# Optimization experiments

Measured on AMD Instinct MI355X. Metric: run time of the kernel, lower is better.

The kernel has to match this reference:

```python
import jax, jax.numpy as jnp
import numpy as np

B, D_IN, D_H = 16384, 512, 1024


def _glorot(key, out_d, in_d):
    lim = 1.0 / np.sqrt(in_d)
    return jax.random.uniform(key, (out_d, in_d), minval=-lim, maxval=lim, dtype=jnp.float32)


def setup_inputs() -> dict:
    key = jax.random.key(0)
    ks = jax.random.split(key, 16)
    inp = {
        "x_t": jax.random.normal(ks[0], (B, D_IN), dtype=jnp.float32),
        "delta_t": jax.random.uniform(ks[1], (B, 1), dtype=jnp.float32),
        "h_prev": jax.random.normal(ks[2], (B, D_H), dtype=jnp.float32),
        # torch nn.Linear weights are [out, in]; y = x @ W.T
        "W_sh": _glorot(ks[3], D_H, D_H),
        "W_sx": _glorot(ks[4], D_H, D_IN),
        "W_st": _glorot(ks[5], D_H, 1),
        "b_s": jnp.zeros((D_H,), jnp.float32),
        "WTh": _glorot(ks[6], D_H, D_H),
        "WTx": _glorot(ks[7], D_H, D_IN),
        "WTs": _glorot(ks[8], D_H, D_H),
        "b_T": jnp.zeros((D_H,), jnp.float32),
        "W_rh": _glorot(ks[9], D_H, D_H),
        "W_rx": _glorot(ks[10], D_H, D_IN),
        "b_r": jnp.zeros((D_H,), jnp.float32),
        "W_zh": _glorot(ks[11], D_H, D_H),
        "W_zx": _glorot(ks[12], D_H, D_IN),
        "b_z": jnp.zeros((D_H,), jnp.float32),
        "W_h": _glorot(ks[13], D_H, D_H),
        "W_x": _glorot(ks[14], D_H, D_IN),
        "b": jnp.zeros((D_H,), jnp.float32),
    }
    return inp


def reference(x_t, delta_t, h_prev,
              W_sh, W_sx, W_st, b_s,
              WTh, WTx, WTs, b_T,
              W_rh, W_rx, b_r,
              W_zh, W_zx, b_z,
              W_h, W_x, b):
    lin = lambda x, W: x @ W.T  # nn.Linear(bias=False)
    s_t = jnp.tanh(lin(h_prev, W_sh) + lin(x_t, W_sx) + lin(delta_t, W_st) + b_s)
    T_t = jax.nn.sigmoid(lin(h_prev, WTh) + lin(x_t, WTx) + lin(s_t, WTs) + b_T)
    r_t = jax.nn.sigmoid(lin(h_prev, W_rh) + lin(x_t, W_rx) + b_r)
    z_t = jax.nn.sigmoid(lin(h_prev, W_zh) + lin(x_t, W_zx) + b_z)
    h_tilde = jnp.tanh(lin(r_t * h_prev, W_h) + lin(x_t, W_x) + b)
    h_t = (1.0 - z_t) * (T_t * h_prev) + z_t * h_tilde
    return h_t
```

## Files before the change

kernel.cpp:

```cpp
#include <hip/hip_runtime.h>
#include <stdint.h>

#define AS1 __attribute__((address_space(1)))
#define AS3 __attribute__((address_space(3)))

typedef unsigned short US;
typedef __bf16 bf16x8 __attribute__((ext_vector_type(8)));
typedef float f32x4 __attribute__((ext_vector_type(4)));
typedef int intx4 __attribute__((ext_vector_type(4)));

static constexpr int Bsz = 16384;
static constexpr int DIN = 512;
static constexpr int DH  = 1024;
static constexpr int LDA = 2560;
static constexpr int LDR = 1536;

__device__ __forceinline__ US f2bf(float f) {
  unsigned u = __float_as_uint(f);
  u += 0x7fffu + ((u >> 16) & 1u);
  return (US)(u >> 16);
}
__device__ __forceinline__ float bf2f(US u) { return __uint_as_float(((unsigned)u) << 16); }
__device__ __forceinline__ float sigm(float x) { return 1.f / (1.f + __expf(-x)); }
__device__ __forceinline__ float tanh_f(float x) { return 1.f - 2.f / (1.f + __expf(2.f * x)); }

__device__ __forceinline__ intx4 dsr128(unsigned addr) {
  intx4 r;
  asm volatile("ds_read_b128 %0, %1" : "=v"(r) : "v"(addr));
  return r;
}

#define SBAR  asm volatile("s_barrier")
#define SB0   __builtin_amdgcn_sched_barrier(0)
#define LGKM0 { asm volatile("s_waitcnt lgkmcnt(0)"); __builtin_amdgcn_sched_barrier(0); }

__global__ void pack_A(const float* __restrict__ h, const float* __restrict__ x,
                       US* __restrict__ Ab, US* __restrict__ RHx) {
  const int total = Bsz * 384;
  for (int idx = blockIdx.x * blockDim.x + threadIdx.x; idx < total;
       idx += gridDim.x * blockDim.x) {
    int row = idx / 384;
    int c = (idx - row * 384) * 4;
    const float* src = (c < DH) ? (h + (size_t)row * DH + c)
                                : (x + (size_t)row * DIN + (c - DH));
    float4 v = *(const float4*)src;
    ushort4 o;
    o.x = f2bf(v.x); o.y = f2bf(v.y); o.z = f2bf(v.z); o.w = f2bf(v.w);
    *(ushort4*)(Ab + (size_t)row * LDA + c) = o;
    if (c >= DH) *(ushort4*)(RHx + (size_t)row * LDR + c) = o;
  }
}

struct WSlot { const float* src; US* dst; int n4; int ksh; int ld; int co; };
struct WBatch { WSlot s[11]; };
__global__ void conv_w(WBatch b) {
  WSlot sl = b.s[blockIdx.y];
  const int mask = (1 << sl.ksh) - 1;
  for (int i = blockIdx.x * blockDim.x + threadIdx.x; i < sl.n4;
       i += gridDim.x * blockDim.x) {
    float4 v = *(const float4*)(sl.src + (size_t)i * 4);
    ushort4 o;
    o.x = f2bf(v.x); o.y = f2bf(v.y); o.z = f2bf(v.z); o.w = f2bf(v.w);
    int r = i >> sl.ksh;
    int cc = (i & mask) * 4;
    *(ushort4*)(sl.dst + (size_t)r * sl.ld + sl.co + cc) = o;
  }
}

template <int EPI, int NBLK>
__global__ __launch_bounds__(512, 2) void gemm8(
    const US* __restrict__ A, int lda,
    const US* __restrict__ W, int ldw, int nt,
    const float* __restrict__ bias0, const float* __restrict__ bias1,
    const float* __restrict__ bias2,
    const void* aux0, const void* aux1, const void* aux2,
    void* out0, int ldo0, void* out1, void* out2) {
  __shared__ __align__(16) US As[2][256 * 64];
  __shared__ __align__(16) US Bs[2][256 * 64];

  const int tid  = threadIdx.x;
  const int lane = tid & 63;
  const int w    = tid >> 6;
  const int wr   = w >> 2;
  const int wc   = w & 3;
  const int quad = lane >> 4, l15 = lane & 15;
  const int sw8  = l15 & 7;
  const int lrow = lane >> 3;
  const int scc  = (lane & 7) ^ (lrow & 7);

  const int p = blockIdx.x;
  const int c = p & 7, q = p >> 3;
  const int nIdx = q % NBLK, mIdx = c * 8 + q / NBLK;
  const int mBase = mIdx * 256, nBase = nIdx * 256;

  f32x4 acc[8][4];
#pragma unroll
  for (int i = 0; i < 8; i++)
#pragma unroll
    for (int j = 0; j < 4; j++) acc[i][j] = f32x4{0.f, 0.f, 0.f, 0.f};

  const unsigned aBase = (unsigned)(uintptr_t)&As[0][0];
  const unsigned bBase = (unsigned)(uintptr_t)&Bs[0][0];
  const unsigned arB = (unsigned)((wr * 128 + l15) * 128);
  const unsigned brB = (unsigned)((wc * 64 + l15) * 128);
  const unsigned kc0 = (unsigned)((quad ^ sw8) * 16);

  const size_t aRowS = (size_t)(mBase + w * 8 + lrow) * lda;
  const size_t wRowS = (size_t)(nBase + w * 8 + lrow) * ldw;
  const int sccOff = scc * 8;

#define STAGE_A(d, hh, co)                                                       \
  { const US* g = A + aRowS + (size_t)(hh) * 128 * lda + (co) + sccOff;          \
    __builtin_amdgcn_global_load_lds((AS1 const void*)g,                         \
        (AS3 void*)&As[d][((hh)*128 + w * 8) * 64], 16, 0, 0);                   \
    __builtin_amdgcn_global_load_lds((AS1 const void*)(g + (size_t)64 * lda),    \
        (AS3 void*)&As[d][((hh)*128 + 64 + w * 8) * 64], 16, 0, 0); }
#define STAGE_B(d, hh, co)                                                       \
  { const US* g = W + wRowS + (size_t)(hh) * 128 * ldw + (co) + sccOff;          \
    __builtin_amdgcn_global_load_lds((AS1 const void*)g,                         \
        (AS3 void*)&Bs[d][((hh)*128 + w * 8) * 64], 16, 0, 0);                   \
    __builtin_amdgcn_global_load_lds((AS1 const void*)(g + (size_t)64 * ldw),    \
        (AS3 void*)&Bs[d][((hh)*128 + 64 + w * 8) * 64], 16, 0, 0); }

#define READ_A(mh)                                                               \
  _Pragma("unroll")                                                              \
  for (int i = 0; i < 4; ++i)                                                    \
    _Pragma("unroll")                                                            \
    for (int ks = 0; ks < 2; ++ks)                                               \
      af[i][ks] = dsr128(aC + arB + (mh)*8192u + (unsigned)i * 2048u +           \
                         (kc0 ^ (unsigned)(ks << 6)));
#define READ_B(BSET, nh)                                                         \
  _Pragma("unroll")                                                              \
  for (int j = 0; j < 2; ++j)                                                    \
    _Pragma("unroll")                                                            \
    for (int ks = 0; ks < 2; ++ks)                                               \
      BSET[j][ks] = dsr128(bC + brB + (nh)*4096u + (unsigned)j * 2048u +         \
                           (kc0 ^ (unsigned)(ks << 6)));
#define MFMA_Q(mh, BSET, nh)                                                     \
  _Pragma("unroll")                                                              \
  for (int ks = 0; ks < 2; ++ks)                                                 \
    _Pragma("unroll")                                                            \
    for (int i = 0; i < 4; ++i)                                                  \
      _Pragma("unroll")                                                          \
      for (int j = 0; j < 2; ++j)                                                \
        acc[(mh)*4 + i][(nh)*2 + j] = __builtin_amdgcn_mfma_f32_16x16x32_bf16(   \
            __builtin_bit_cast(bf16x8, af[i][ks]),                               \
            __builtin_bit_cast(bf16x8, BSET[j][ks]),                             \
            acc[(mh)*4 + i][(nh)*2 + j], 0, 0, 0);

  STAGE_B(0, 0, 0); STAGE_B(0, 1, 0); STAGE_A(0, 0, 0); STAGE_A(0, 1, 0);
  STAGE_B(1, 0, 64); STAGE_B(1, 1, 64); STAGE_A(1, 0, 64); STAGE_A(1, 1, 64);
  asm volatile("s_waitcnt vmcnt(8)");
  SBAR; SB0;

  intx4 af[4][2], b0[2][2], b1[2][2];
  int cur = 0;

  for (int t = 0; t < nt; ++t, cur ^= 1) {
    const unsigned aC = aBase + (unsigned)cur * 32768u;
    const unsigned bC = bBase + (unsigned)cur * 32768u;
    const bool haveS = (t + 2 < nt);
    const int co2 = (t + 2) * 64;
    READ_A(0);
    READ_B(b0, 0);
    SBAR; SB0;
    LGKM0;
    __builtin_amdgcn_s_setprio(1);
    MFMA_Q(0, b0, 0);
    __builtin_amdgcn_s_setprio(0);
    SBAR; SB0;
    READ_B(b1, 1);
    SBAR; SB0;
    LGKM0;
    __builtin_amdgcn_s_setprio(1);
    MFMA_Q(0, b1, 1);
    __builtin_amdgcn_s_setprio(0);
    SBAR; SB0;
    READ_A(1);
    if (haveS) { STAGE_B(cur, 0, co2); STAGE_B(cur, 1, co2); }
    SBAR; SB0;
    LGKM0;
    __builtin_amdgcn_s_setprio(1);
    MFMA_Q(1, b0, 0);
    __builtin_amdgcn_s_setprio(0);
    SBAR; SB0;
    if (haveS) { STAGE_A(cur, 0, co2); STAGE_A(cur, 1, co2); }
    SBAR; SB0;
    __builtin_amdgcn_s_setprio(1);
    MFMA_Q(1, b1, 1);
    __builtin_amdgcn_s_setprio(0);
    if (t + 1 < nt) {
      if (haveS) { asm volatile("s_waitcnt vmcnt(8)"); }
      else       { asm volatile("s_waitcnt vmcnt(0)"); }
      SBAR; SB0;
    }
  }
#undef STAGE_A
#undef STAGE_B
#undef READ_A
#undef READ_B
#undef MFMA_Q

#pragma unroll
  for (int im = 0; im < 8; ++im) {
#pragma unroll
    for (int jn = 0; jn < 4; ++jn) {
      const int col = nBase + wc * 64 + jn * 16 + l15;
      if constexpr (EPI == 0) {
        const int g = nIdx >> 2;
        const int colg = col & 1023;
        const float* bp = (g == 0) ? bias0 : (g == 1) ? bias1 : bias2;
        const float bv = bp[colg];
        const float* delta = (const float*)aux0;
        const float* wst   = (const float*)aux1;
        const float* hp    = (const float*)aux2;
#pragma unroll
        for (int r = 0; r < 4; ++r) {
          const int row = mBase + wr * 128 + im * 16 + quad * 4 + r;
          float v = acc[im][jn][r] + bv;
          if (g == 0) {
            v += delta[row] * wst[colg];
            ((US*)out0)[(size_t)row * ldo0 + colg] = f2bf(tanh_f(v));
          } else if (g == 1) {
            float rr = sigm(v);
            ((US*)out1)[(size_t)row * LDR + colg] =
                f2bf(rr * hp[(size_t)row * DH + colg]);
          } else {
            ((US*)out2)[(size_t)row * DH + colg] = f2bf(sigm(v));
          }
        }
      } else if constexpr (EPI == 3) {
        const float bv = bias0[col];
#pragma unroll
        for (int r = 0; r < 4; ++r) {
          const int row = mBase + wr * 128 + im * 16 + quad * 4 + r;
          float v = acc[im][jn][r] + bv;
          ((US*)out0)[(size_t)row * ldo0 + col] = f2bf(tanh_f(v));
        }
      } else {
        const float bv = bias0[col];
        const float* hp = (const float*)aux0;
        const US* Zp = (const US*)aux1;
        const US* Hp = (const US*)aux2;
#pragma unroll
        for (int r = 0; r < 4; ++r) {
          const int row = mBase + wr * 128 + im * 16 + quad * 4 + r;
          float v = acc[im][jn][r] + bv;
          float T = sigm(v);
          size_t o = (size_t)row * DH + col;
          float z = bf2f(Zp[o]), ht = bf2f(Hp[o]);
          float h = hp[o];
          ((float*)out0)[(size_t)row * ldo0 + col] = (1.f - z) * (T * h) + z * ht;
        }
      }
    }
  }
}

extern "C" void kernel_launch(void* const* d_in, const int* in_sizes, int n_in,
                              void* d_out, int out_size, void* d_ws, size_t ws_size,
                              hipStream_t stream) {
  const float* x_t   = (const float*)d_in[0];
  const float* delta = (const float*)d_in[1];
  const float* h_prev= (const float*)d_in[2];
  const float* W_sh  = (const float*)d_in[3];
  const float* W_sx  = (const float*)d_in[4];
  const float* W_st  = (const float*)d_in[5];
  const float* b_s   = (const float*)d_in[6];
  const float* WTh   = (const float*)d_in[7];
  const float* WTx   = (const float*)d_in[8];
  const float* WTs   = (const float*)d_in[9];
  const float* b_T   = (const float*)d_in[10];
  const float* W_rh  = (const float*)d_in[11];
  const float* W_rx  = (const float*)d_in[12];
  const float* b_r   = (const float*)d_in[13];
  const float* W_zh  = (const float*)d_in[14];
  const float* W_zx  = (const float*)d_in[15];
  const float* b_z   = (const float*)d_in[16];
  const float* W_h   = (const float*)d_in[17];
  const float* W_x   = (const float*)d_in[18];
  const float* b_    = (const float*)d_in[19];
  float* out = (float*)d_out;

  char* ws = (char*)d_ws;
  US* Ab  = (US*)ws;              size_t off = (size_t)Bsz * LDA * 2;
  US* RH  = (US*)(ws + off);      off += (size_t)Bsz * LDR * 2;
  US* Zb  = (US*)(ws + off);      off += (size_t)Bsz * DH * 2;
  US* HTb = (US*)(ws + off);      off += (size_t)Bsz * DH * 2;
  US* bWsrz = (US*)(ws + off);    off += (size_t)3072 * 1536 * 2;
  US* bWT   = (US*)(ws + off);    off += (size_t)DH * 2560 * 2;
  US* bWh   = (US*)(ws + off);    off += (size_t)DH * 1536 * 2;

  pack_A<<<dim3(8192), 256, 0, stream>>>(h_prev, x_t, Ab, RH);
  WBatch wb;
  const int n4h = DH * DH / 4, n4x = DH * DIN / 4;
  US* bWr = bWsrz + (size_t)1024 * 1536;
  US* bWz = bWsrz + (size_t)2048 * 1536;
  wb.s[0]  = {W_sh, bWsrz, n4h, 8, 1536, 0};
  wb.s[1]  = {W_sx, bWsrz, n4x, 7, 1536, 1024};
  wb.s[2]  = {W_rh, bWr,   n4h, 8, 1536, 0};
  wb.s[3]  = {W_rx, bWr,   n4x, 7, 1536, 1024};
  wb.s[4]  = {W_zh, bWz,   n4h, 8, 1536, 0};
  wb.s[5]  = {W_zx, bWz,   n4x, 7, 1536, 1024};
  wb.s[6]  = {WTh,  bWT,   n4h, 8, 2560, 0};
  wb.s[7]  = {WTx,  bWT,   n4x, 7, 2560, 1024};
  wb.s[8]  = {WTs,  bWT,   n4h, 8, 2560, 1536};
  wb.s[9]  = {W_h,  bWh,   n4h, 8, 1536, 0};
  wb.s[10] = {W_x,  bWh,   n4x, 7, 1536, 1024};
  conv_w<<<dim3(512, 11), 256, 0, stream>>>(wb);

  gemm8<0, 12><<<dim3(768), 512, 0, stream>>>(
      Ab, LDA, bWsrz, 1536, 24, b_s, b_r, b_z,
      delta, W_st, h_prev, (void*)(Ab + 1536), LDA, (void*)RH, (void*)Zb);
  gemm8<3, 4><<<dim3(256), 512, 0, stream>>>(
      RH, LDR, bWh, 1536, 24, b_, nullptr, nullptr,
      nullptr, nullptr, nullptr, (void*)HTb, DH, nullptr, nullptr);
  gemm8<4, 4><<<dim3(256), 512, 0, stream>>>(
      Ab, LDA, bWT, 2560, 40, b_T, nullptr, nullptr,
      h_prev, Zb, HTb, (void*)out, DH, nullptr, nullptr);
}
```

Measured before the change: 688.9 us.

## Replace interleaved prefetch-distance-2 GEMM pipeline with simple one-ahead double buffering

The main loop is restructured. Each iteration now issues the next tile's global-to-LDS loads into the other buffer, reads all of the A and B fragments at once into separate register sets, runs all the MFMAs, and then waits for vmcnt(0) before a single barrier. This replaces the earlier schedule, which ran two tiles ahead and split each iteration into four phases with barriers between them. The fewer barriers and waits are meant to cut synchronisation overhead, at the cost of a shorter prefetch distance and more fragment registers (af0/af1), which could lower occupancy or expose memory latency.

New measurement: 672.8 us. 1.02x faster.

```diff
diff --git a/kernel.cpp b/kernel.cpp
--- a/kernel.cpp
+++ b/kernel.cpp
@@ -30,9 +30,10 @@
   return r;
 }
 
-#define SBAR  asm volatile("s_barrier")
+#define SBAR  asm volatile("s_barrier" ::: "memory")
 #define SB0   __builtin_amdgcn_sched_barrier(0)
-#define LGKM0 { asm volatile("s_waitcnt lgkmcnt(0)"); __builtin_amdgcn_sched_barrier(0); }
+#define LGKM0 { asm volatile("s_waitcnt lgkmcnt(0)" ::: "memory"); __builtin_amdgcn_sched_barrier(0); }
+#define VM0   { asm volatile("s_waitcnt vmcnt(0)" ::: "memory"); __builtin_amdgcn_sched_barrier(0); }
 
 __global__ void pack_A(const float* __restrict__ h, const float* __restrict__ x,
                        US* __restrict__ Ab, US* __restrict__ RHx) {
@@ -122,12 +123,12 @@
     __builtin_amdgcn_global_load_lds((AS1 const void*)(g + (size_t)64 * ldw),    \
         (AS3 void*)&Bs[d][((hh)*128 + 64 + w * 8) * 64], 16, 0, 0); }
 
-#define READ_A(mh)                                                               \
+#define READ_A(AF, mh)                                                           \
   _Pragma("unroll")                                                              \
   for (int i = 0; i < 4; ++i)                                                    \
     _Pragma("unroll")                                                            \
     for (int ks = 0; ks < 2; ++ks)                                               \
-      af[i][ks] = dsr128(aC + arB + (mh)*8192u + (unsigned)i * 2048u +           \
+      AF[i][ks] = dsr128(aC + arB + (mh)*8192u + (unsigned)i * 2048u +           \
                          (kc0 ^ (unsigned)(ks << 6)));
 #define READ_B(BSET, nh)                                                         \
   _Pragma("unroll")                                                              \
@@ -136,7 +137,7 @@
     for (int ks = 0; ks < 2; ++ks)                                               \
       BSET[j][ks] = dsr128(bC + brB + (nh)*4096u + (unsigned)j * 2048u +         \
                            (kc0 ^ (unsigned)(ks << 6)));
-#define MFMA_Q(mh, BSET, nh)                                                     \
+#define MFMA_Q(AF, mh, BSET, nh)                                                 \
   _Pragma("unroll")                                                              \
   for (int ks = 0; ks < 2; ++ks)                                                 \
     _Pragma("unroll")                                                            \
@@ -144,56 +145,40 @@
       _Pragma("unroll")                                                          \
       for (int j = 0; j < 2; ++j)                                                \
         acc[(mh)*4 + i][(nh)*2 + j] = __builtin_amdgcn_mfma_f32_16x16x32_bf16(   \
-            __builtin_bit_cast(bf16x8, af[i][ks]),                               \
+            __builtin_bit_cast(bf16x8, AF[i][ks]),                               \
             __builtin_bit_cast(bf16x8, BSET[j][ks]),                             \
             acc[(mh)*4 + i][(nh)*2 + j], 0, 0, 0);
 
-  STAGE_B(0, 0, 0); STAGE_B(0, 1, 0); STAGE_A(0, 0, 0); STAGE_A(0, 1, 0);
-  STAGE_B(1, 0, 64); STAGE_B(1, 1, 64); STAGE_A(1, 0, 64); STAGE_A(1, 1, 64);
-  asm volatile("s_waitcnt vmcnt(8)");
+  STAGE_A(0, 0, 0); STAGE_A(0, 1, 0); STAGE_B(0, 0, 0); STAGE_B(0, 1, 0);
+  VM0;
   SBAR; SB0;
 
-  intx4 af[4][2], b0[2][2], b1[2][2];
+  intx4 af0[4][2], af1[4][2], b0[2][2], b1[2][2];
   int cur = 0;
 
   for (int t = 0; t < nt; ++t, cur ^= 1) {
     const unsigned aC = aBase + (unsigned)cur * 32768u;
     const unsigned bC = bBase + (unsigned)cur * 32768u;
-    const bool haveS = (t + 2 < nt);
-    const int co2 = (t + 2) * 64;
-    READ_A(0);
+    const int nxt = cur ^ 1;
+    const int co1 = (t + 1) * 64;
+    if (t + 1 < nt) {
+      STAGE_A(nxt, 0, co1); STAGE_A(nxt, 1, co1);
+      STAGE_B(nxt, 0, co1); STAGE_B(nxt, 1, co1);
+    }
+    READ_A(af0, 0);
+    READ_A(af1, 1);
     READ_B(b0, 0);
-    SBAR; SB0;
+    READ_B(b1, 1);
     LGKM0;
     __builtin_amdgcn_s_setprio(1);
-    MFMA_Q(0, b0, 0);
+    MFMA_Q(af0, 0, b0, 0);
+    MFMA_Q(af0, 0, b1, 1);
+    MFMA_Q(af1, 1, b0, 0);
+    MFMA_Q(af1, 1, b1, 1);
     __builtin_amdgcn_s_setprio(0);
+    SB0;
+    if (t + 1 < nt) { VM0; }
     SBAR; SB0;
-    READ_B(b1, 1);
-    SBAR; SB0;
-    LGKM0;
-    __builtin_amdgcn_s_setprio(1);
-    MFMA_Q(0, b1, 1);
-    __builtin_amdgcn_s_setprio(0);
-    SBAR; SB0;
-    READ_A(1);
-    if (haveS) { STAGE_B(cur, 0, co2); STAGE_B(cur, 1, co2); }
-    SBAR; SB0;
-    LGKM0;
-    __builtin_amdgcn_s_setprio(1);
-    MFMA_Q(1, b0, 0);
-    __builtin_amdgcn_s_setprio(0);
-    SBAR; SB0;
-    if (haveS) { STAGE_A(cur, 0, co2); STAGE_A(cur, 1, co2); }
-    SBAR; SB0;
-    __builtin_amdgcn_s_setprio(1);
-    MFMA_Q(1, b1, 1);
-    __builtin_amdgcn_s_setprio(0);
-    if (t + 1 < nt) {
-      if (haveS) { asm volatile("s_waitcnt vmcnt(8)"); }
-      else       { asm volatile("s_waitcnt vmcnt(0)"); }
-      SBAR; SB0;
-    }
   }
 #undef STAGE_A
 #undef STAGE_B
```
